# Kernel tuning notes

Measured on AMD Instinct MI355X. Metric: run time of the kernel, lower is better.

Reference implementation:

```python
import jax, jax.numpy as jnp
import numpy as np

WINDOW = (7, 7)
SHIFT = (3, 3)
NUM_HEADS = 4
DIM = 128


def _rel_pos_index():
    wh, ww = WINDOW
    coords = np.stack(np.meshgrid(np.arange(wh), np.arange(ww), indexing='ij'))  # [2,wh,ww]
    cf = coords.reshape(2, -1)                    # [2, N]
    rc = (cf[:, :, None] - cf[:, None, :]).transpose(1, 2, 0)  # [N,N,2]
    rc[:, :, 0] += wh - 1
    rc[:, :, 1] += ww - 1
    rc[:, :, 0] *= 2 * ww - 1
    return jnp.asarray(rc.sum(-1).reshape(-1))    # [N*N] int


def _attn_mask_np(pH, pW, sh):
    # Static-shape shift mask (host-side numpy; constant under jit).
    wh, ww = WINDOW
    m = np.zeros((pH, pW))
    h_slices = ((0, pH - wh), (pH - wh, pH - sh[0]), (pH - sh[0], pH))
    w_slices = ((0, pW - ww), (pW - ww, pW - sh[1]), (pW - sh[1], pW))
    cnt = 0
    for hs in h_slices:
        for ws in w_slices:
            m[hs[0]:hs[1], ws[0]:ws[1]] = cnt
            cnt += 1
    m = m.reshape(pH // wh, wh, pW // ww, ww).transpose(0, 2, 1, 3).reshape(-1, wh * ww)
    diff = m[:, None, :] - m[:, :, None]          # [num_windows, N, N]
    return jnp.asarray(np.where(diff != 0, -100.0, 0.0), dtype=np.float32)


def setup_inputs() -> dict:
    key = jax.random.key(0)
    ks = jax.random.split(key, 9)
    B, H, W, C = 32, 56, 56, DIM
    return {
        'input_q': jax.random.normal(ks[0], (B, H, W, C), jnp.float32),
        'input_k': jax.random.normal(ks[1], (B, H, W, C), jnp.float32),
        'input_v': jax.random.normal(ks[2], (B, H, W, C), jnp.float32),
        'q_weight': jax.random.normal(ks[3], (C, C), jnp.float32) * 0.05,
        'q_bias': jnp.zeros((C,), jnp.float32),
        'k_weight': jax.random.normal(ks[4], (C, C), jnp.float32) * 0.05,
        'k_bias': jnp.zeros((C,), jnp.float32),
        'v_weight': jax.random.normal(ks[5], (C, C), jnp.float32) * 0.05,
        'v_bias': jnp.zeros((C,), jnp.float32),
        'proj_weight': jax.random.normal(ks[6], (C, C), jnp.float32) * 0.05,
        'proj_bias': jnp.zeros((C,), jnp.float32),
        'rpb_table': jax.random.normal(ks[7], ((2 * WINDOW[0] - 1) * (2 * WINDOW[1] - 1), NUM_HEADS), jnp.float32) * 0.02,
    }


def reference(input_q, input_k, input_v, q_weight, q_bias, k_weight, k_bias,
              v_weight, v_bias, proj_weight, proj_bias, rpb_table):
    B, H, W, C = input_q.shape
    wh, ww = WINDOW
    pad_b = (wh - H % wh) % wh
    pad_r = (ww - W % ww) % ww
    pad = lambda t: jnp.pad(t, ((0, 0), (0, pad_b), (0, pad_r), (0, 0)))
    qx, kx, vx = pad(input_q), pad(input_k), pad(input_v)
    pad_H, pad_W = H + pad_b, W + pad_r
    sh = [0 if wh >= pad_H else SHIFT[0], 0 if ww >= pad_W else SHIFT[1]]
    if sum(sh) > 0:
        roll = lambda t: jnp.roll(t, (-sh[0], -sh[1]), axis=(1, 2))
        qx, kx, vx = roll(qx), roll(kx), roll(vx)
    nWh, nWw = pad_H // wh, pad_W // ww
    num_windows = nWh * nWw
    N = wh * ww

    def part(t):  # [B,pH,pW,C] -> [B*num_windows, N, C]
        t = t.reshape(B, nWh, wh, nWw, ww, C).transpose(0, 1, 3, 2, 4, 5)
        return t.reshape(B * num_windows, N, C)

    qx, kx, vx = part(qx), part(kx), part(vx)
    hd = C // NUM_HEADS

    def heads(x, w, b):  # linear + split heads -> [BW, nH, N, hd]
        return (x @ w.T + b).reshape(-1, N, NUM_HEADS, hd).transpose(0, 2, 1, 3)

    q = heads(qx, q_weight, q_bias) * (hd ** -0.5)
    k = heads(kx, k_weight, k_bias)
    v = heads(vx, v_weight, v_bias)

    attn = jnp.einsum('whqd,whkd->whqk', q, k)    # [BW, nH, N, N]
    rpb = rpb_table[_rel_pos_index()].reshape(N, N, NUM_HEADS).transpose(2, 0, 1)[None]
    attn = attn + rpb
    if sum(sh) > 0:
        mask = _attn_mask_np(pad_H, pad_W, sh)    # [num_windows, N, N]
        attn = attn.reshape(B, num_windows, NUM_HEADS, N, N) + mask[None, :, None]
        attn = attn.reshape(B * num_windows, NUM_HEADS, N, N)
    attn = jax.nn.softmax(attn, axis=-1)

    x = jnp.einsum('whqk,whkd->whqd', attn, v).transpose(0, 2, 1, 3).reshape(B * num_windows, N, C)
    x = x @ proj_weight.T + proj_bias
    x = x.reshape(B, nWh, nWw, wh, ww, C).transpose(0, 1, 3, 2, 4, 5).reshape(B, pad_H, pad_W, C)
    if sum(sh) > 0:
        x = jnp.roll(x, (sh[0], sh[1]), axis=(1, 2))
    return x[:, :H, :W, :]
```

## Files before the change

kernel.cpp:

```cpp
#include <hip/hip_runtime.h>
#include <hip/hip_bf16.h>

typedef __attribute__((ext_vector_type(8))) short s16x8;
typedef __attribute__((ext_vector_type(4))) float f32x4;
typedef __attribute__((ext_vector_type(16))) float f32x16;
typedef __attribute__((ext_vector_type(2))) unsigned int u32x2;
typedef __attribute__((ext_vector_type(4))) unsigned int u32x4;

#define MFMA16(a, b, c) __builtin_amdgcn_mfma_f32_16x16x32_bf16((a), (b), (c), 0, 0, 0)
#define MFMA32(a, b, c) __builtin_amdgcn_mfma_f32_32x32x16_bf16((a), (b), (c), 0, 0, 0)
#define LOG2E 1.4426950408889634f

static __device__ __forceinline__ unsigned int pk2(float a, float b) {
  union { __hip_bfloat162 h2; unsigned int u; } cv;
  cv.h2 = __float22bfloat162_rn(make_float2(a, b));
  return cv.u;
}
static __device__ __forceinline__ int div7(int x) { return (x * 9363) >> 16; }
static __device__ __forceinline__ int swz256(int row, int byteoff) {
  return row * 256 + (byteoff ^ ((row & 7) << 4));
}
static __device__ __forceinline__ int swz128(int row, int byteoff) {
  return row * 128 + (byteoff ^ ((row & 7) << 4));
}

__global__ void swin_prep(const float* __restrict__ wq, const float* __restrict__ wk,
                          const float* __restrict__ wv, const float* __restrict__ wp,
                          const float* __restrict__ rpb_table,
                          unsigned short* __restrict__ wsW, float* __restrict__ rpbm) {
  int idx = blockIdx.x * 256 + threadIdx.x;
  if (idx < 65536) {
    int t = idx >> 14, loc = idx & 16383;
    const float* s = (t == 0) ? wq : (t == 1) ? wk : (t == 2) ? wv : wp;
    union { __hip_bfloat16 h; unsigned short u; } cv;
    cv.h = __float2bfloat16(s[loc]);
    wsW[idx] = cv.u;
  } else {
    int k = idx - 65536;
    int c = k >> 14;
    int h = (k >> 12) & 3;
    int i = (k >> 6) & 63, j = k & 63;
    float val;
    if (j >= 49) val = -1e30f;
    else if (i >= 49) val = 0.f;
    else {
      int yi = div7(i), xi = i - yi * 7;
      int yj = div7(j), xj = j - yj * 7;
      int ridx = (yi - yj + 6) * 13 + (xi - xj + 6);
      val = rpb_table[ridx * 4 + h];
      int cwi = c >> 1, cwj = c & 1;
      int rgi = (cwi ? (yi < 4 ? 3 : 6) : 0) + (cwj ? (xi < 4 ? 1 : 2) : 0);
      int rgj = (cwi ? (yj < 4 ? 3 : 6) : 0) + (cwj ? (xj < 4 ? 1 : 2) : 0);
      if (rgi != rgj) val -= 100.f;
      val *= LOG2E;
    }
    rpbm[k] = val;
  }
}

__global__ __launch_bounds__(512, 6) void swin_main(
    const float* __restrict__ xq, const float* __restrict__ xk, const float* __restrict__ xv,
    const float* __restrict__ bq, const float* __restrict__ bk, const float* __restrict__ bv,
    const float* __restrict__ bp, const unsigned short* __restrict__ wsW,
    const float* __restrict__ rpbm, float* __restrict__ out) {
  __shared__ __align__(16) char sm[49152];

  const int tid = threadIdx.x;
  const int lane = tid & 63;
  const int wv_ = tid >> 6;
  const int l15 = lane & 15;
  const int lg = lane >> 4;
  const int kgrp = lg * 8;
  const int rsub = lg * 4;
  const int l31 = lane & 31;
  const int hi = lane >> 5;

  const int bid = blockIdx.x;
  const int b = bid >> 6;
  const int widx = bid & 63;
  const int wi = widx >> 3, wj = widx & 7;
  const long obase = (long)b * 56 * 56 * 128;
  const int mcase = ((wi == 7) ? 2 : 0) + ((wj == 7) ? 1 : 0);

  const int xrow = tid >> 3;
  const int xk16 = (tid & 7) << 4;
  long xoff = -1;
  if (xrow < 49) {
    int ty = div7(xrow), tx = xrow - ty * 7;
    int ih = wi * 7 + ty + 3; if (ih >= 56) ih -= 56;
    int iw = wj * 7 + tx + 3; if (iw >= 56) iw -= 56;
    xoff = obase + (long)((ih * 56 + iw) * 128 + xk16);
  }
  {
    float ra[16], rb[16], rc[16];
#pragma unroll
    for (int i = 0; i < 16; ++i) { ra[i] = 0.f; rb[i] = 0.f; rc[i] = 0.f; }
    if (xoff >= 0) {
#pragma unroll
      for (int q = 0; q < 4; ++q) {
        f32x4 v = *(const f32x4*)(xq + xoff + q * 4);
        ra[q*4+0]=v[0]; ra[q*4+1]=v[1]; ra[q*4+2]=v[2]; ra[q*4+3]=v[3];
      }
#pragma unroll
      for (int q = 0; q < 4; ++q) {
        f32x4 v = *(const f32x4*)(xk + xoff + q * 4);
        rb[q*4+0]=v[0]; rb[q*4+1]=v[1]; rb[q*4+2]=v[2]; rb[q*4+3]=v[3];
      }
#pragma unroll
      for (int q = 0; q < 4; ++q) {
        f32x4 v = *(const f32x4*)(xv + xoff + q * 4);
        rc[q*4+0]=v[0]; rc[q*4+1]=v[1]; rc[q*4+2]=v[2]; rc[q*4+3]=v[3];
      }
    }
    auto wrx = [&](int base, float* r) {
      unsigned int w[8];
#pragma unroll
      for (int i = 0; i < 8; ++i) w[i] = pk2(r[2*i], r[2*i+1]);
      u32x4 a = {w[0], w[1], w[2], w[3]};
      u32x4 bb = {w[4], w[5], w[6], w[7]};
      *(u32x4*)(sm + base + swz256(xrow, xk16 * 2)) = a;
      *(u32x4*)(sm + base + swz256(xrow, xk16 * 2 + 16)) = bb;
    };
    wrx(0, ra);
    wrx(16384, rb);
    wrx(32768, rc);
  }
  __syncthreads();

  const float QSCALE = 0.17677669529663687f * LOG2E;
  unsigned int qpk[4][2], kpk[4][2], vpk[4][2];
  {
    const int nrow = wv_ * 16 + l15;
    {
      s16x8 afr[4];
#pragma unroll
      for (int kt = 0; kt < 4; ++kt)
        afr[kt] = *(const s16x8*)(wsW + nrow * 128 + kt * 32 + kgrp);
      f32x4 bv4 = *(const f32x4*)(bq + wv_ * 16 + rsub);
#pragma unroll
      for (int tt = 0; tt < 4; ++tt) {
        f32x4 acc = {0.f, 0.f, 0.f, 0.f};
#pragma unroll
        for (int kt = 0; kt < 4; ++kt) {
          s16x8 bfr = *(const s16x8*)(sm + swz256(tt * 16 + l15, (kt * 32 + kgrp) * 2));
          acc = MFMA16(afr[kt], bfr, acc);
        }
        qpk[tt][0] = pk2(acc[0] * QSCALE + bv4[0] * QSCALE, acc[1] * QSCALE + bv4[1] * QSCALE);
        qpk[tt][1] = pk2(acc[2] * QSCALE + bv4[2] * QSCALE, acc[3] * QSCALE + bv4[3] * QSCALE);
      }
    }
    {
      s16x8 afr[4];
#pragma unroll
      for (int kt = 0; kt < 4; ++kt)
        afr[kt] = *(const s16x8*)(wsW + 16384 + nrow * 128 + kt * 32 + kgrp);
      f32x4 bv4 = *(const f32x4*)(bk + wv_ * 16 + rsub);
#pragma unroll
      for (int tt = 0; tt < 4; ++tt) {
        f32x4 acc = {0.f, 0.f, 0.f, 0.f};
#pragma unroll
        for (int kt = 0; kt < 4; ++kt) {
          s16x8 bfr = *(const s16x8*)(sm + 16384 + swz256(tt * 16 + l15, (kt * 32 + kgrp) * 2));
          acc = MFMA16(afr[kt], bfr, acc);
        }
        kpk[tt][0] = pk2(acc[0] + bv4[0], acc[1] + bv4[1]);
        kpk[tt][1] = pk2(acc[2] + bv4[2], acc[3] + bv4[3]);
      }
    }
    {
      s16x8 bfrw[4];
#pragma unroll
      for (int kt = 0; kt < 4; ++kt)
        bfrw[kt] = *(const s16x8*)(wsW + 32768 + nrow * 128 + kt * 32 + kgrp);
      float bval = bv[nrow];
#pragma unroll
      for (int mt = 0; mt < 4; ++mt) {
        f32x4 acc = {0.f, 0.f, 0.f, 0.f};
#pragma unroll
        for (int kt = 0; kt < 4; ++kt) {
          s16x8 afr = *(const s16x8*)(sm + 32768 + swz256(mt * 16 + l15, (kt * 32 + kgrp) * 2));
          acc = MFMA16(afr, bfrw[kt], acc);
        }
        vpk[mt][0] = pk2(acc[0] + bval, acc[1] + bval);
        vpk[mt][1] = pk2(acc[2] + bval, acc[3] + bval);
      }
    }
  }
  __syncthreads();

#pragma unroll
  for (int tt = 0; tt < 4; ++tt) {
    u32x2 w = {qpk[tt][0], qpk[tt][1]};
    *(u32x2*)(sm + swz256(tt * 16 + l15, 2 * (wv_ * 16 + rsub))) = w;
  }
#pragma unroll
  for (int tt = 0; tt < 4; ++tt) {
    u32x2 w = {kpk[tt][0], kpk[tt][1]};
    *(u32x2*)(sm + 16384 + swz256(tt * 16 + l15, 2 * (wv_ * 16 + rsub))) = w;
  }
#pragma unroll
  for (int mt = 0; mt < 4; ++mt) {
    u32x2 w = {vpk[mt][0], vpk[mt][1]};
    *(u32x2*)(sm + 32768 + swz128(wv_ * 16 + l15, 2 * (mt * 16 + rsub))) = w;
  }
  __syncthreads();

  const int h = wv_ & 3;
  const int half = wv_ >> 2;
  const int coff = h * 32;
  unsigned int pu[2][4][2];
  f32x16 O;
  {
    const float* rpbm_h = rpbm + (((mcase << 2) + h) << 12) + (half * 32 + l31) * 64 + 4 * hi;
    f32x16 S[2];
#pragma unroll
    for (int t = 0; t < 2; ++t)
#pragma unroll
      for (int g = 0; g < 4; ++g) {
        f32x4 rv = *(const f32x4*)(rpbm_h + t * 32 + g * 8);
        S[t][g*4+0] = rv[0]; S[t][g*4+1] = rv[1];
        S[t][g*4+2] = rv[2]; S[t][g*4+3] = rv[3];
      }
    s16x8 qfr[2], kfr[2][2];
#pragma unroll
    for (int s = 0; s < 2; ++s) {
      qfr[s] = *(const s16x8*)(sm + swz256(half * 32 + l31, 2 * (coff + s * 16 + hi * 8)));
#pragma unroll
      for (int t = 0; t < 2; ++t)
        kfr[t][s] = *(const s16x8*)(sm + 16384 + swz256(t * 32 + l31, 2 * (coff + s * 16 + hi * 8)));
    }
#pragma unroll
    for (int s = 0; s < 2; ++s) {
      S[0] = MFMA32(kfr[0][s], qfr[s], S[0]);
      S[1] = MFMA32(kfr[1][s], qfr[s], S[1]);
    }
    float m = S[0][0];
#pragma unroll
    for (int t = 0; t < 2; ++t)
#pragma unroll
      for (int r = 0; r < 16; ++r) m = fmaxf(m, S[t][r]);
    m = fmaxf(m, __shfl_xor(m, 32));
    float sum = 0.f;
#pragma unroll
    for (int t = 0; t < 2; ++t)
#pragma unroll
      for (int r = 0; r < 16; ++r) { float e = exp2f(S[t][r] - m); S[t][r] = e; sum += e; }
    sum += __shfl_xor(sum, 32);
    float inv = 1.0f / sum;
#pragma unroll
    for (int t = 0; t < 2; ++t)
#pragma unroll
      for (int g = 0; g < 4; ++g) {
        pu[t][g][0] = pk2(S[t][g*4+0] * inv, S[t][g*4+1] * inv);
        pu[t][g][1] = pk2(S[t][g*4+2] * inv, S[t][g*4+3] * inv);
      }
    O = (f32x16)0.f;
#pragma unroll
    for (int s = 0; s < 4; ++s) {
      const int t = s >> 1, gb = (s & 1) * 2;
      unsigned int own0 = pu[t][gb + hi][0], own1 = pu[t][gb + hi][1];
      unsigned int po0 = __shfl_xor(pu[t][gb + 1 - hi][0], 32);
      unsigned int po1 = __shfl_xor(pu[t][gb + 1 - hi][1], 32);
      union { u32x4 u; s16x8 s; } pf;
      pf.u = hi ? (u32x4){po0, po1, own0, own1} : (u32x4){own0, own1, po0, po1};
      s16x8 vfr = *(const s16x8*)(sm + 32768 + swz128(coff + l31, 2 * (s * 16 + hi * 8)));
      O = MFMA32(vfr, pf.s, O);
    }
  }
  __syncthreads();

#pragma unroll
  for (int g = 0; g < 4; ++g) {
    u32x2 w = {pk2(O[g*4+0], O[g*4+1]), pk2(O[g*4+2], O[g*4+3])};
    *(u32x2*)(sm + swz256(half * 32 + l31, 2 * (coff + g * 8 + 4 * hi))) = w;
  }
  __syncthreads();

  {
    const int nrow = wv_ * 16 + l15;
    s16x8 afr[4];
#pragma unroll
    for (int kt = 0; kt < 4; ++kt)
      afr[kt] = *(const s16x8*)(wsW + 49152 + nrow * 128 + kt * 32 + kgrp);
    f32x4 bv4 = *(const f32x4*)(bp + wv_ * 16 + rsub);
#pragma unroll
    for (int tt = 0; tt < 4; ++tt) {
      f32x4 acc = {0.f, 0.f, 0.f, 0.f};
#pragma unroll
      for (int kt = 0; kt < 4; ++kt) {
        s16x8 bfr = *(const s16x8*)(sm + swz256(tt * 16 + l15, (kt * 32 + kgrp) * 2));
        acc = MFMA16(afr[kt], bfr, acc);
      }
      int tok = tt * 16 + l15;
      if (tok < 49) {
        int ty = div7(tok), tx = tok - ty * 7;
        int oh = wi * 7 + ty + 3; if (oh >= 56) oh -= 56;
        int ow = wj * 7 + tx + 3; if (ow >= 56) ow -= 56;
        f32x4 res = {acc[0] + bv4[0], acc[1] + bv4[1], acc[2] + bv4[2], acc[3] + bv4[3]};
        *(f32x4*)(out + obase + (oh * 56 + ow) * 128 + wv_ * 16 + rsub) = res;
      }
    }
  }
}

extern "C" void kernel_launch(void* const* d_in, const int* in_sizes, int n_in,
                              void* d_out, int out_size, void* d_ws, size_t ws_size,
                              hipStream_t stream) {
  const float* xq = (const float*)d_in[0];
  const float* xk = (const float*)d_in[1];
  const float* xv = (const float*)d_in[2];
  const float* wq = (const float*)d_in[3];
  const float* bq = (const float*)d_in[4];
  const float* wk = (const float*)d_in[5];
  const float* bk = (const float*)d_in[6];
  const float* wv = (const float*)d_in[7];
  const float* bv = (const float*)d_in[8];
  const float* wp = (const float*)d_in[9];
  const float* bp = (const float*)d_in[10];
  const float* rpb = (const float*)d_in[11];

  unsigned short* wsW = (unsigned short*)d_ws;
  float* rpbm = (float*)((char*)d_ws + 131072);

  swin_prep<<<512, 256, 0, stream>>>(wq, wk, wv, wp, rpb, wsW, rpbm);

  float* out = (float*)d_out;
  swin_main<<<2048, 512, 0, stream>>>(xq, xk, xv, bq, bk, bv, bp, wsW, rpbm, out);
}
```

Measured before the change: 82.90 us.

## Compute per-head Q/K projections directly in MFMA32 fragment layout, skip LDS round-trip

New measurement: 108.9 us. +31.3%, slower.

```diff
diff --git a/kernel.cpp b/kernel.cpp
--- a/kernel.cpp
+++ b/kernel.cpp
@@ -58,7 +58,7 @@
   }
 }
 
-__global__ __launch_bounds__(512, 6) void swin_main(
+__global__ __launch_bounds__(512, 4) void swin_main(
     const float* __restrict__ xq, const float* __restrict__ xk, const float* __restrict__ xv,
     const float* __restrict__ bq, const float* __restrict__ bk, const float* __restrict__ bv,
     const float* __restrict__ bp, const unsigned short* __restrict__ wsW,
@@ -112,104 +112,77 @@
         rc[q*4+0]=v[0]; rc[q*4+1]=v[1]; rc[q*4+2]=v[2]; rc[q*4+3]=v[3];
       }
     }
-    auto wrx = [&](int base, float* r) {
+    auto wrx = [&](int base, const float* r) {
       unsigned int w[8];
 #pragma unroll
       for (int i = 0; i < 8; ++i) w[i] = pk2(r[2*i], r[2*i+1]);
       u32x4 a = {w[0], w[1], w[2], w[3]};
-      u32x4 bb = {w[4], w[5], w[6], w[7]};
+      u32x4 bb2 = {w[4], w[5], w[6], w[7]};
       *(u32x4*)(sm + base + swz256(xrow, xk16 * 2)) = a;
-      *(u32x4*)(sm + base + swz256(xrow, xk16 * 2 + 16)) = bb;
+      *(u32x4*)(sm + base + swz256(xrow, xk16 * 2 + 16)) = bb2;
     };
-    wrx(0, ra);
-    wrx(16384, rb);
-    wrx(32768, rc);
+    wrx(0, ra); wrx(16384, rb); wrx(32768, rc);
   }
   __syncthreads();
 
   const float QSCALE = 0.17677669529663687f * LOG2E;
-  unsigned int qpk[4][2], kpk[4][2], vpk[4][2];
-  {
-    const int nrow = wv_ * 16 + l15;
-    {
-      s16x8 afr[4];
-#pragma unroll
-      for (int kt = 0; kt < 4; ++kt)
-        afr[kt] = *(const s16x8*)(wsW + nrow * 128 + kt * 32 + kgrp);
-      f32x4 bv4 = *(const f32x4*)(bq + wv_ * 16 + rsub);
-#pragma unroll
-      for (int tt = 0; tt < 4; ++tt) {
-        f32x4 acc = {0.f, 0.f, 0.f, 0.f};
-#pragma unroll
-        for (int kt = 0; kt < 4; ++kt) {
-          s16x8 bfr = *(const s16x8*)(sm + swz256(tt * 16 + l15, (kt * 32 + kgrp) * 2));
-          acc = MFMA16(afr[kt], bfr, acc);
-        }
-        qpk[tt][0] = pk2(acc[0] * QSCALE + bv4[0] * QSCALE, acc[1] * QSCALE + bv4[1] * QSCALE);
-        qpk[tt][1] = pk2(acc[2] * QSCALE + bv4[2] * QSCALE, acc[3] * QSCALE + bv4[3] * QSCALE);
-      }
-    }
-    {
-      s16x8 afr[4];
-#pragma unroll
-      for (int kt = 0; kt < 4; ++kt)
-        afr[kt] = *(const s16x8*)(wsW + 16384 + nrow * 128 + kt * 32 + kgrp);
-      f32x4 bv4 = *(const f32x4*)(bk + wv_ * 16 + rsub);
-#pragma unroll
-      for (int tt = 0; tt < 4; ++tt) {
-        f32x4 acc = {0.f, 0.f, 0.f, 0.f};
-#pragma unroll
-        for (int kt = 0; kt < 4; ++kt) {
-          s16x8 bfr = *(const s16x8*)(sm + 16384 + swz256(tt * 16 + l15, (kt * 32 + kgrp) * 2));
-          acc = MFMA16(afr[kt], bfr, acc);
-        }
-        kpk[tt][0] = pk2(acc[0] + bv4[0], acc[1] + bv4[1]);
-        kpk[tt][1] = pk2(acc[2] + bv4[2], acc[3] + bv4[3]);
-      }
-    }
-    {
-      s16x8 bfrw[4];
-#pragma unroll
-      for (int kt = 0; kt < 4; ++kt)
-        bfrw[kt] = *(const s16x8*)(wsW + 32768 + nrow * 128 + kt * 32 + kgrp);
-      float bval = bv[nrow];
-#pragma unroll
-      for (int mt = 0; mt < 4; ++mt) {
-        f32x4 acc = {0.f, 0.f, 0.f, 0.f};
-#pragma unroll
-        for (int kt = 0; kt < 4; ++kt) {
-          s16x8 afr = *(const s16x8*)(sm + 32768 + swz256(mt * 16 + l15, (kt * 32 + kgrp) * 2));
-          acc = MFMA16(afr, bfrw[kt], acc);
-        }
-        vpk[mt][0] = pk2(acc[0] + bval, acc[1] + bval);
-        vpk[mt][1] = pk2(acc[2] + bval, acc[3] + bval);
-      }
-    }
-  }
-  __syncthreads();
-
-#pragma unroll
-  for (int tt = 0; tt < 4; ++tt) {
-    u32x2 w = {qpk[tt][0], qpk[tt][1]};
-    *(u32x2*)(sm + swz256(tt * 16 + l15, 2 * (wv_ * 16 + rsub))) = w;
-  }
-#pragma unroll
-  for (int tt = 0; tt < 4; ++tt) {
-    u32x2 w = {kpk[tt][0], kpk[tt][1]};
-    *(u32x2*)(sm + 16384 + swz256(tt * 16 + l15, 2 * (wv_ * 16 + rsub))) = w;
-  }
-#pragma unroll
-  for (int mt = 0; mt < 4; ++mt) {
-    u32x2 w = {vpk[mt][0], vpk[mt][1]};
-    *(u32x2*)(sm + 32768 + swz128(wv_ * 16 + l15, 2 * (mt * 16 + rsub))) = w;
-  }
-  __syncthreads();
-
   const int h = wv_ & 3;
   const int half = wv_ >> 2;
   const int coff = h * 32;
+  const int nrow = wv_ * 16 + l15;
+
+  unsigned int vpk[4][2];
+  {
+    s16x8 bfrw[4];
+#pragma unroll
+    for (int kt = 0; kt < 4; ++kt)
+      bfrw[kt] = *(const s16x8*)(wsW + 32768 + nrow * 128 + kt * 32 + kgrp);
+    float bval = bv[nrow];
+#pragma unroll
+    for (int mt = 0; mt < 4; ++mt) {
+      f32x4 acc = {0.f, 0.f, 0.f, 0.f};
+#pragma unroll
+      for (int kt = 0; kt < 4; ++kt) {
+        s16x8 afr = *(const s16x8*)(sm + 32768 + swz256(mt * 16 + l15, (kt * 32 + kgrp) * 2));
+        acc = MFMA16(afr, bfrw[kt], acc);
+      }
+      vpk[mt][0] = pk2(acc[0] + bval, acc[1] + bval);
+      vpk[mt][1] = pk2(acc[2] + bval, acc[3] + bval);
+    }
+  }
+
+  f32x16 DQ = (f32x16)0.f, DK0 = (f32x16)0.f, DK1 = (f32x16)0.f;
+#pragma unroll
+  for (int ks = 0; ks < 8; ++ks) {
+    const int kb = ks * 16 + hi * 8;
+    s16x8 aQ = *(const s16x8*)(wsW + (coff + l31) * 128 + kb);
+    s16x8 bQ = *(const s16x8*)(sm + swz256(half * 32 + l31, 2 * kb));
+    DQ = MFMA32(aQ, bQ, DQ);
+    s16x8 aK = *(const s16x8*)(wsW + 16384 + (coff + l31) * 128 + kb);
+    s16x8 bK0 = *(const s16x8*)(sm + 16384 + swz256(l31, 2 * kb));
+    DK0 = MFMA32(aK, bK0, DK0);
+    s16x8 bK1 = *(const s16x8*)(sm + 16384 + swz256(32 + l31, 2 * kb));
+    DK1 = MFMA32(aK, bK1, DK1);
+  }
+
+  auto mkfrag = [&](const f32x16& D, const float* bias, float scale, int s) -> s16x8 {
+    f32x4 b0 = *(const f32x4*)(bias + coff + 16 * s + 4 * hi);
+    f32x4 b1 = *(const f32x4*)(bias + coff + 16 * s + 8 + 4 * hi);
+    unsigned int g0w0 = pk2((D[8*s+0] + b0[0]) * scale, (D[8*s+1] + b0[1]) * scale);
+    unsigned int g0w1 = pk2((D[8*s+2] + b0[2]) * scale, (D[8*s+3] + b0[3]) * scale);
+    unsigned int g1w0 = pk2((D[8*s+4] + b1[0]) * scale, (D[8*s+5] + b1[1]) * scale);
+    unsigned int g1w1 = pk2((D[8*s+6] + b1[2]) * scale, (D[8*s+7] + b1[3]) * scale);
+    unsigned int s0 = hi ? g0w0 : g1w0, s1 = hi ? g0w1 : g1w1;
+    unsigned int r0 = __shfl_xor(s0, 32), r1 = __shfl_xor(s1, 32);
+    union { u32x4 u; s16x8 s8; } f;
+    f.u = hi ? (u32x4){r0, r1, g1w0, g1w1} : (u32x4){g0w0, g0w1, r0, r1};
+    return f.s8;
+  };
+  s16x8 qf0 = mkfrag(DQ, bq, QSCALE, 0), qf1 = mkfrag(DQ, bq, QSCALE, 1);
+  s16x8 kf00 = mkfrag(DK0, bk, 1.f, 0), kf01 = mkfrag(DK0, bk, 1.f, 1);
+  s16x8 kf10 = mkfrag(DK1, bk, 1.f, 0), kf11 = mkfrag(DK1, bk, 1.f, 1);
+
   unsigned int pu[2][4][2];
-  f32x16 O;
   {
     const float* rpbm_h = rpbm + (((mcase << 2) + h) << 12) + (half * 32 + l31) * 64 + 4 * hi;
     f32x16 S[2];
@@ -221,19 +194,10 @@
         S[t][g*4+0] = rv[0]; S[t][g*4+1] = rv[1];
         S[t][g*4+2] = rv[2]; S[t][g*4+3] = rv[3];
       }
-    s16x8 qfr[2], kfr[2][2];
-#pragma unroll
-    for (int s = 0; s < 2; ++s) {
-      qfr[s] = *(const s16x8*)(sm + swz256(half * 32 + l31, 2 * (coff + s * 16 + hi * 8)));
-#pragma unroll
-      for (int t = 0; t < 2; ++t)
-        kfr[t][s] = *(const s16x8*)(sm + 16384 + swz256(t * 32 + l31, 2 * (coff + s * 16 + hi * 8)));
-    }
-#pragma unroll
-    for (int s = 0; s < 2; ++s) {
-      S[0] = MFMA32(kfr[0][s], qfr[s], S[0]);
-      S[1] = MFMA32(kfr[1][s], qfr[s], S[1]);
-    }
+    S[0] = MFMA32(kf00, qf0, S[0]);
+    S[0] = MFMA32(kf01, qf1, S[0]);
+    S[1] = MFMA32(kf10, qf0, S[1]);
+    S[1] = MFMA32(kf11, qf1, S[1]);
     float m = S[0][0];
 #pragma unroll
     for (int t = 0; t < 2; ++t)
@@ -254,7 +218,18 @@
         pu[t][g][0] = pk2(S[t][g*4+0] * inv, S[t][g*4+1] * inv);
         pu[t][g][1] = pk2(S[t][g*4+2] * inv, S[t][g*4+3] * inv);
       }
-    O = (f32x16)0.f;
+  }
+  __syncthreads();
+
+#pragma unroll
+  for (int mt = 0; mt < 4; ++mt) {
+    u32x2 w = {vpk[mt][0], vpk[mt][1]};
+    *(u32x2*)(sm + 32768 + swz128(nrow, 2 * (mt * 16 + rsub))) = w;
+  }
+  __syncthreads();
+
+  {
+    f32x16 O = (f32x16)0.f;
 #pragma unroll
     for (int s = 0; s < 4; ++s) {
       const int t = s >> 1, gb = (s & 1) * 2;
@@ -266,18 +241,15 @@
       s16x8 vfr = *(const s16x8*)(sm + 32768 + swz128(coff + l31, 2 * (s * 16 + hi * 8)));
       O = MFMA32(vfr, pf.s, O);
     }
+#pragma unroll
+    for (int g = 0; g < 4; ++g) {
+      u32x2 w = {pk2(O[g*4+0], O[g*4+1]), pk2(O[g*4+2], O[g*4+3])};
+      *(u32x2*)(sm + swz256(half * 32 + l31, 2 * (coff + g * 8 + 4 * hi))) = w;
+    }
   }
   __syncthreads();
 
-#pragma unroll
-  for (int g = 0; g < 4; ++g) {
-    u32x2 w = {pk2(O[g*4+0], O[g*4+1]), pk2(O[g*4+2], O[g*4+3])};
-    *(u32x2*)(sm + swz256(half * 32 + l31, 2 * (coff + g * 8 + 4 * hi))) = w;
-  }
-  __syncthreads();
-
-  {
-    const int nrow = wv_ * 16 + l15;
+  {
     s16x8 afr[4];
 #pragma unroll
     for (int kt = 0; kt < 4; ++kt)
```
